# Kernel optimization log

Hardware: AMD Instinct MI355X
Metric: run time of the kernel (lower is better)

## Reference

```python
import jax, jax.numpy as jnp
import numpy as np

DT = 0.1
DN = ('NCHW', 'OIHW', 'NCHW')

LAP = jnp.array([[1., 2., 1.], [2., -12., 2.], [1., 2., 1.]], jnp.float32)
SOBEL_X = jnp.array([[-1., 0., 1.], [-2., 0., 2.], [-1., 0., 1.]], jnp.float32)
LAP_K = (LAP / 12.0)[None, None]  # [1,1,3,3], zero-padded laplacian kernel


def conv_lap(x):
    # 3x3 laplacian/12 conv with zero padding=1 on a single-channel map
    return jax.lax.conv_general_dilated(x, LAP_K, (1, 1), ((1, 1), (1, 1)), dimension_numbers=DN)


def conv1x1(x, w, b=None):
    # w: [O, C]
    y = jnp.einsum('bchw,oc->bohw', x, w)
    if b is not None:
        y = y + b[None, :, None, None]
    return y


def avg_pool5(x):
    # torch avg_pool2d(5,1,2) with count_include_pad=True -> always divide by 25
    s = jax.lax.reduce_window(x, 0.0, jax.lax.add, (1, 1, 5, 5), (1, 1, 1, 1),
                              [(0, 0), (0, 0), (2, 2), (2, 2)])
    return s / 25.0


def min_pool3(x):
    # -maxpool(-x) in torch == min-pool with +inf padding
    return jax.lax.reduce_window(x, jnp.inf, jax.lax.min, (1, 1, 3, 3), (1, 1, 1, 1),
                                 [(0, 0), (0, 0), (1, 1), (1, 1)])


def perception(x):
    # reduced_perception(x, 0): depthwise circular 3x3 conv with [sobel_x, sobel_x.T, lap]
    B, C, H, W = x.shape
    filters = jnp.stack([SOBEL_X, SOBEL_X.T, LAP])        # [3,3,3]
    k = jnp.tile(filters, (C, 1, 1))[:, None]              # [3C,1,3,3]; per-channel groups of 3
    xp = jnp.pad(x, ((0, 0), (0, 0), (1, 1), (1, 1)), mode='wrap')
    obs = jax.lax.conv_general_dilated(xp, k, (1, 1), 'VALID',
                                       feature_group_count=C, dimension_numbers=DN)
    return jnp.concatenate([x, obs], axis=1)               # [B, 4C, H, W]


def setup_inputs() -> dict:
    key = jax.random.key(0)
    ks = jax.random.split(key, 10)
    B, C, H, W = 16, 21, 256, 256
    hidden_n, gene_size = 96, 3
    return {
        'x': jax.random.uniform(ks[0], (B, C, H, W), jnp.float32),
        'rand_noise': jax.random.uniform(ks[1], (B, 1, H, W), jnp.float32),
        'w1_w': jax.random.normal(ks[2], (hidden_n, 4 * C), jnp.float32) * 0.05,
        'w1_b': jax.random.normal(ks[3], (hidden_n,), jnp.float32) * 0.02,
        'w2_w': jax.random.normal(ks[4], (gene_size, hidden_n), jnp.float32) * 0.05,
        'slow_w': jax.random.normal(ks[5], (3, 5), jnp.float32) * 0.1,
        'slow_b': jax.random.normal(ks[6], (3,), jnp.float32) * 0.02,
        'mod_w': jax.random.normal(ks[7], (3, 3), jnp.float32) * 0.1,
        'mod_b': jax.random.normal(ks[8], (3,), jnp.float32) * 0.02,
        'alpha': jnp.float32(0.1),
        'beta': jnp.float32(0.1),
        'omega': jnp.float32(0.0),
        'K': jnp.float32(0.5),
        'kappa': jnp.float32(0.5),
    }


def reference(x, rand_noise, w1_w, w1_b, w2_w, slow_w, slow_b, mod_w, mod_b,
              alpha, beta, omega, K, kappa):
    # step=0, k=4 -> slow (reaction-diffusion) branch executes; update_rate=0.5
    prefix = x[:, :12]
    gene = x[:, 12:15]
    a = x[:, 15:16]
    b = x[:, 16:17]
    d = x[:, 17:18]

    # slow_perception on rgba + hidden
    alpha_ch = x[:, 3:4]
    eroded = min_pool3(alpha_ch)
    Q = jnp.concatenate([alpha_ch, alpha_ch - eroded, conv_lap(alpha_ch), x[:, 4:6]], axis=1)  # 5 ch
    I = conv1x1(Q, slow_w, slow_b)
    Ia, Ib, Id = I[:, 0:1], I[:, 1:2], I[:, 2:3]

    # discrete reaction-diffusion update
    new_a = a + DT * (-alpha * a + omega * b + K * conv_lap(a) + Ia)
    new_b = b + DT * (-alpha * b - omega * a + K * conv_lap(b) + Ib)
    new_d = d + DT * (-beta * d + kappa * conv_lap(d) + Id)

    # local consensus update
    a_avg = avg_pool5(new_a)
    b_avg = avg_pool5(new_b)
    rho = jnp.sqrt(a_avg ** 2 + b_avg ** 2 + 1e-6)
    a_avg = a_avg / rho
    b_avg = b_avg / rho
    new_a = new_a + DT * (a_avg - new_a)
    new_b = new_b + DT * (b_avg - new_b)

    # ring attractor phases (variable naming follows the source's swapped unpack)
    phase = jnp.sqrt(new_a ** 2 + new_b ** 2 + 1e-6)  # local amplitude
    amplitude = jnp.arctan2(new_b, new_a)             # local angle
    a, b, d = new_a, new_b, new_d

    mod = conv1x1(jnp.concatenate([a, b, d], axis=1), mod_w, mod_b)

    # gene update MLP over full perception
    y = conv1x1(jax.nn.relu(conv1x1(perception(x), w1_w, w1_b)), w2_w)

    update_mask = jnp.floor(rand_noise + 0.5)
    xmp = jnp.pad(x[:, 3:4], ((0, 0), (0, 0), (1, 1), (1, 1)), mode='wrap')
    life = (jax.lax.reduce_window(xmp, -jnp.inf, jax.lax.max, (1, 1, 3, 3), (1, 1, 1, 1),
                                  'VALID') > 0.1).astype(x.dtype)
    new_gene = gene + y * update_mask * life

    x_final = jnp.concatenate([prefix, new_gene, a, b, d, mod], axis=1)
    return x_final, phase, amplitude
```

## Files before the change

### kernel.cpp

```cpp
#include <hip/hip_runtime.h>
#include <math.h>

#define HH 256
#define WW 256
#define CC 21
#define BB 16
#define HW (HH*WW)
#define CHW (CC*HW)
#define PHASE_OFF (BB*CHW)
#define AMP_OFF (PHASE_OFF + BB*HW)

static constexpr float DT = 0.1f;

typedef short short8 __attribute__((ext_vector_type(8)));
typedef float floatx4 __attribute__((ext_vector_type(4)));

__device__ __forceinline__ unsigned f2bf_bits(float f) {
    unsigned u = __builtin_bit_cast(unsigned, f);
    return (u + 0x7fffu + ((u >> 16) & 1u)) >> 16;
}
__device__ __forceinline__ float bf2f(short s) {
    unsigned u = ((unsigned)(unsigned short)s) << 16;
    return __builtin_bit_cast(float, u);
}

__global__ __launch_bounds__(256)
void k0_prep(const float* __restrict__ w1w, const float* __restrict__ w1b,
             const float* __restrict__ w2w,
             short* __restrict__ weff, float4* __restrict__ w2b)
{
    const float SX[9] = {-1.f, 0.f, 1.f, -2.f, 0.f, 2.f, -1.f, 0.f, 1.f};
    const float SY[9] = {-1.f, -2.f, -1.f, 0.f, 0.f, 0.f, 1.f, 2.f, 1.f};
    const float LP[9] = {1.f, 2.f, 1.f, 2.f, -12.f, 2.f, 1.f, 2.f, 1.f};
    const int i = blockIdx.x * 256 + threadIdx.x;
    if (i < 9 * 96 * 32) {
        const int s = i / (96 * 32);
        const int rem = i - s * 96 * 32;
        const int n = rem >> 5, c = rem & 31;
        float v = 0.f;
        if (c < 21) {
            v = w1w[n * 84 + c] * ((s == 4) ? 1.f : 0.f)
              + w1w[n * 84 + 21 + 3 * c + 0] * SX[s]
              + w1w[n * 84 + 21 + 3 * c + 1] * SY[s]
              + w1w[n * 84 + 21 + 3 * c + 2] * LP[s];
        }
        weff[i] = (short)f2bf_bits(v);
    } else if (i < 9 * 96 * 32 + 96) {
        const int n = i - 9 * 96 * 32;
        w2b[n] = make_float4(w2w[n], w2w[96 + n], w2w[192 + n], w1b[n]);
    }
}

__global__ __launch_bounds__(256)
void k12_react(const float* __restrict__ x,
               const float* __restrict__ slow_w, const float* __restrict__ slow_b,
               const float* __restrict__ mod_w, const float* __restrict__ mod_b,
               const float* __restrict__ alpha_p, const float* __restrict__ beta_p,
               const float* __restrict__ omega_p, const float* __restrict__ K_p,
               const float* __restrict__ kappa_p,
               float* __restrict__ out)
{
    __shared__ float t[6][14][38];
    __shared__ float na[12][36], nb[12][36];
    __shared__ float ha[12][32], hb[12][32];

    const int tx = threadIdx.x, ty = threadIdx.y;
    const int bb = blockIdx.z;
    const int X0 = blockIdx.x * 32, Y0 = blockIdx.y * 8;
    const int tid = ty * 32 + tx;

    const float alpha = alpha_p[0], beta = beta_p[0], omega = omega_p[0];
    const float Kc = K_p[0], kappa = kappa_p[0];

    const float* xb = x + (size_t)bb * CHW;
    for (int i = tid; i < 532; i += 256) {
        const int r = i / 38, c = i - r * 38;
        const int gy = Y0 + r - 3, gx = X0 + c - 3;
        const bool inb = (gy >= 0) && (gy < HH) && (gx >= 0) && (gx < WW);
        const int off = gy * WW + gx;
        t[0][r][c] = inb ? xb[3  * HW + off] : 0.f;
        t[1][r][c] = inb ? xb[4  * HW + off] : 0.f;
        t[2][r][c] = inb ? xb[5  * HW + off] : 0.f;
        t[3][r][c] = inb ? xb[15 * HW + off] : 0.f;
        t[4][r][c] = inb ? xb[16 * HW + off] : 0.f;
        t[5][r][c] = inb ? xb[17 * HW + off] : 0.f;
    }
    __syncthreads();

    for (int i = tid; i < 432; i += 256) {
        const int r2 = i / 36, c2 = i - r2 * 36;
        const int gy = Y0 + r2 - 2, gx = X0 + c2 - 2;
        float va = 0.f, vb = 0.f;
        if (gy >= 0 && gy < HH && gx >= 0 && gx < WW) {
            const int lr = r2 + 1, lc = c2 + 1;
            float lap3 = 0.f, lapA = 0.f, lapB = 0.f, emin = INFINITY;
            #pragma unroll
            for (int dy = -1; dy <= 1; dy++) {
                #pragma unroll
                for (int dx = -1; dx <= 1; dx++) {
                    const float lw = ((dy == 0 && dx == 0) ? -12.f
                                     : ((dy == 0 || dx == 0) ? 2.f : 1.f)) * (1.f / 12.f);
                    const float v3 = t[0][lr + dy][lc + dx];
                    lap3 = fmaf(lw, v3, lap3);
                    lapA = fmaf(lw, t[3][lr + dy][lc + dx], lapA);
                    lapB = fmaf(lw, t[4][lr + dy][lc + dx], lapB);
                    const bool nin = (gy + dy >= 0) && (gy + dy < HH) && (gx + dx >= 0) && (gx + dx < WW);
                    emin = fminf(emin, nin ? v3 : INFINITY);
                }
            }
            const float Q0 = t[0][lr][lc];
            const float Q1 = Q0 - emin, Q2 = lap3;
            const float Q3 = t[1][lr][lc], Q4 = t[2][lr][lc];
            const float I0 = slow_b[0] + slow_w[0] * Q0 + slow_w[1] * Q1 + slow_w[2] * Q2 + slow_w[3] * Q3 + slow_w[4] * Q4;
            const float I1 = slow_b[1] + slow_w[5] * Q0 + slow_w[6] * Q1 + slow_w[7] * Q2 + slow_w[8] * Q3 + slow_w[9] * Q4;
            const float a = t[3][lr][lc], b = t[4][lr][lc];
            va = a + DT * (-alpha * a + omega * b + Kc * lapA + I0);
            vb = b + DT * (-alpha * b - omega * a + Kc * lapB + I1);
        }
        na[r2][c2] = va;
        nb[r2][c2] = vb;
    }
    __syncthreads();

    for (int i = tid; i < 384; i += 256) {
        const int r = i >> 5, c = i & 31;
        float sa = 0.f, sb = 0.f;
        #pragma unroll
        for (int dx = 0; dx < 5; dx++) { sa += na[r][c + dx]; sb += nb[r][c + dx]; }
        ha[r][c] = sa; hb[r][c] = sb;
    }
    __syncthreads();

    const int gy = Y0 + ty, gx = X0 + tx;
    const int lr = ty + 3, lc = tx + 3;

    float sa = 0.f, sb = 0.f;
    #pragma unroll
    for (int dy = 0; dy < 5; dy++) { sa += ha[ty + dy][tx]; sb += hb[ty + dy][tx]; }
    sa *= (1.f / 25.f); sb *= (1.f / 25.f);
    const float rho = sqrtf(sa * sa + sb * sb + 1e-6f);
    const float an = sa / rho, bn = sb / rho;
    const float a0 = na[ty + 2][tx + 2], b0 = nb[ty + 2][tx + 2];
    const float A2 = a0 + DT * (an - a0);
    const float B2 = b0 + DT * (bn - b0);

    float lapD = 0.f, lap3 = 0.f, emin = INFINITY;
    #pragma unroll
    for (int dy = -1; dy <= 1; dy++)
        #pragma unroll
        for (int dx = -1; dx <= 1; dx++) {
            const float lw = ((dy == 0 && dx == 0) ? -12.f
                             : ((dy == 0 || dx == 0) ? 2.f : 1.f)) * (1.f / 12.f);
            lapD = fmaf(lw, t[5][lr + dy][lc + dx], lapD);
            const float v3 = t[0][lr + dy][lc + dx];
            lap3 = fmaf(lw, v3, lap3);
            const bool nin = (gy + dy >= 0) && (gy + dy < HH) && (gx + dx >= 0) && (gx + dx < WW);
            emin = fminf(emin, nin ? v3 : INFINITY);
        }
    const float Q0 = t[0][lr][lc];
    const float I2 = slow_b[2] + slow_w[10] * Q0 + slow_w[11] * (Q0 - emin) + slow_w[12] * lap3
                   + slow_w[13] * t[1][lr][lc] + slow_w[14] * t[2][lr][lc];
    const float d0 = t[5][lr][lc];
    const float nd = d0 + DT * (-beta * d0 + kappa * lapD + I2);

    const float ph = sqrtf(A2 * A2 + B2 * B2 + 1e-6f);
    const float am = atan2f(B2, A2);

    const int po = gy * WW + gx;
    float* ob = out + bb * CHW;
    ob[15 * HW + po] = A2;
    ob[16 * HW + po] = B2;
    ob[17 * HW + po] = nd;
    #pragma unroll
    for (int j = 0; j < 3; j++)
        ob[(18 + j) * HW + po] = mod_b[j] + mod_w[j * 3 + 0] * A2 + mod_w[j * 3 + 1] * B2 + mod_w[j * 3 + 2] * nd;
    out[PHASE_OFF + bb * HW + po] = ph;
    out[AMP_OFF + bb * HW + po] = am;
}

__global__ __launch_bounds__(256, 3)
void k3_gene(const float* __restrict__ x, const float* __restrict__ noise,
             const short* __restrict__ weff, const float4* __restrict__ w2b,
             float* __restrict__ out)
{
    __shared__ __align__(16) short xt[10][34][40];

    const int tx = threadIdx.x, ty = threadIdx.y;
    const int tid = ty * 32 + tx;
    const int w = tid >> 6, lane = tid & 63;
    const int ln = lane & 15, kg = lane >> 4;
    const int bb = blockIdx.z;
    const int X0 = blockIdx.x * 32, Y0 = blockIdx.y * 8;
    const float* xb = x + bb * CHW;

    for (int idx = tid; idx < 340; idx += 256) {
        const int r = idx / 34, cc = idx - r * 34;
        const int gy = (Y0 + r - 1) & (HH - 1);
        const int gxx = (X0 + cc - 1) & (WW - 1);
        const float* src = xb + gy * WW + gxx;
        short* dst = &xt[r][cc][0];
        #pragma unroll
        for (int c = 0; c < 20; c += 2) {
            const unsigned lo = f2bf_bits(src[c * HW]);
            const unsigned hi = f2bf_bits(src[(c + 1) * HW]);
            *(unsigned*)(dst + c) = lo | (hi << 16);
        }
        *(unsigned*)(dst + 20) = f2bf_bits(src[20 * HW]);
        #pragma unroll
        for (int c = 22; c < 40; c += 2) *(unsigned*)(dst + c) = 0u;
    }
    __syncthreads();

    const int gy = Y0 + ty, gx = X0 + tx;
    const int po = gy * WW + gx;
    float* ob = out + bb * CHW;
    const float* xc = xb + po;
    #pragma unroll
    for (int c = 0; c < 12; c++) ob[c * HW + po] = xc[c * HW];
    const float c12 = xc[12 * HW], c13 = xc[13 * HW], c14 = xc[14 * HW];

    float m = -1e30f;
    #pragma unroll
    for (int ky = 0; ky < 3; ky++)
        #pragma unroll
        for (int kx = 0; kx < 3; kx++)
            m = fmaxf(m, bf2f(xt[ty + ky][tx + kx][3]));
    const float life = (m > 0.1f) ? 1.f : 0.f;
    const float g = floorf(noise[bb * HW + po] + 0.5f) * life;

    const short* xtf = &xt[0][0][0];
    int aoff[4];
    #pragma unroll
    for (int mt = 0; mt < 4; mt++)
        aoff[mt] = ((2 * w + (mt >> 1)) * 34 + (mt & 1) * 16 + ln) * 40 + kg * 8;

    float yj0[4] = {0.f, 0.f, 0.f, 0.f};
    float yj1[4] = {0.f, 0.f, 0.f, 0.f};
    float yj2[4] = {0.f, 0.f, 0.f, 0.f};

    #pragma unroll
    for (int pass = 0; pass < 2; pass++) {
        floatx4 acc[4][3];
        #pragma unroll
        for (int mt = 0; mt < 4; mt++)
            #pragma unroll
            for (int nt = 0; nt < 3; nt++)
                acc[mt][nt] = (floatx4){0.f, 0.f, 0.f, 0.f};

        #pragma unroll
        for (int s = 0; s < 9; s++) {
            const int soff = ((s / 3) * 34 + (s % 3)) * 40;
            short8 af[4];
            #pragma unroll
            for (int mt = 0; mt < 4; mt++)
                af[mt] = *(const short8*)(xtf + aoff[mt] + soff);
            short8 bf[3];
            #pragma unroll
            for (int nt = 0; nt < 3; nt++)
                bf[nt] = *(const short8*)(weff + ((size_t)(s * 96 + pass * 48 + nt * 16 + ln)) * 32 + kg * 8);
            #pragma unroll
            for (int nt = 0; nt < 3; nt++)
                #pragma unroll
                for (int mt = 0; mt < 4; mt++)
                    acc[mt][nt] = __builtin_amdgcn_mfma_f32_16x16x32_bf16(bf[nt], af[mt], acc[mt][nt], 0, 0, 0);
        }

        #pragma unroll
        for (int nt = 0; nt < 3; nt++) {
            float4 wb[4];
            #pragma unroll
            for (int r = 0; r < 4; r++)
                wb[r] = w2b[pass * 48 + nt * 16 + kg * 4 + r];
            #pragma unroll
            for (int mt = 0; mt < 4; mt++)
                #pragma unroll
                for (int r = 0; r < 4; r++) {
                    const float h = fmaxf(acc[mt][nt][r] + wb[r].w, 0.f);
                    yj0[mt] = fmaf(h, wb[r].x, yj0[mt]);
                    yj1[mt] = fmaf(h, wb[r].y, yj1[mt]);
                    yj2[mt] = fmaf(h, wb[r].z, yj2[mt]);
                }
        }
    }

    float fy0 = 0.f, fy1 = 0.f, fy2 = 0.f;
    #pragma unroll
    for (int mt = 0; mt < 4; mt++) {
        float t0 = yj0[mt] + __shfl_xor(yj0[mt], 16, 64);
        t0 += __shfl_xor(t0, 32, 64);
        float t1 = yj1[mt] + __shfl_xor(yj1[mt], 16, 64);
        t1 += __shfl_xor(t1, 32, 64);
        float t2 = yj2[mt] + __shfl_xor(yj2[mt], 16, 64);
        t2 += __shfl_xor(t2, 32, 64);
        if (kg == mt) { fy0 = t0; fy1 = t1; fy2 = t2; }
    }

    ob[12 * HW + po] = c12 + fy0 * g;
    ob[13 * HW + po] = c13 + fy1 * g;
    ob[14 * HW + po] = c14 + fy2 * g;
}

extern "C" void kernel_launch(void* const* d_in, const int* in_sizes, int n_in,
                              void* d_out, int out_size, void* d_ws, size_t ws_size,
                              hipStream_t stream)
{
    const float* x      = (const float*)d_in[0];
    const float* noise  = (const float*)d_in[1];
    const float* w1w    = (const float*)d_in[2];
    const float* w1b    = (const float*)d_in[3];
    const float* w2w    = (const float*)d_in[4];
    const float* sloww  = (const float*)d_in[5];
    const float* slowb  = (const float*)d_in[6];
    const float* modw   = (const float*)d_in[7];
    const float* modb   = (const float*)d_in[8];
    const float* alphap = (const float*)d_in[9];
    const float* betap  = (const float*)d_in[10];
    const float* omegap = (const float*)d_in[11];
    const float* Kp     = (const float*)d_in[12];
    const float* kappap = (const float*)d_in[13];
    float* out = (float*)d_out;

    short* weff = (short*)d_ws;
    float4* w2b = (float4*)((char*)d_ws + 55296);

    dim3 blk(32, 8, 1);
    dim3 grd(WW / 32, HH / 8, BB);

    k0_prep<<<dim3(109), dim3(256), 0, stream>>>(w1w, w1b, w2w, weff, w2b);
    k12_react<<<grd, blk, 0, stream>>>(x, sloww, slowb, modw, modb,
                                       alphap, betap, omegap, Kp, kappap, out);
    k3_gene<<<grd, blk, 0, stream>>>(x, noise, weff, w2b, out);
}
```

Before: 307.0 us.

## Merge reaction and gene kernels into one launch with interleaved block roles

The separate reaction-diffusion and gene-MLP kernels become a single kernel. Even and odd blocks take the gene (MFMA) role and the reaction (stencil) role, and the two roles share shared memory through a union. The aim is to run the memory-bound stencil blocks alongside the compute-bound MFMA blocks on the same CUs, and to drop one kernel launch plus the tail gap between the two kernels. In exchange, the merged kernel runs under launch_bounds(256,3) and the reaction blocks allocate the larger union LDS footprint, which could limit occupancy.

```diff
diff --git a/kernel.cpp b/kernel.cpp
--- a/kernel.cpp
+++ b/kernel.cpp
@@ -51,253 +51,250 @@
     }
 }
 
-__global__ __launch_bounds__(256)
-void k12_react(const float* __restrict__ x,
-               const float* __restrict__ slow_w, const float* __restrict__ slow_b,
-               const float* __restrict__ mod_w, const float* __restrict__ mod_b,
-               const float* __restrict__ alpha_p, const float* __restrict__ beta_p,
-               const float* __restrict__ omega_p, const float* __restrict__ K_p,
-               const float* __restrict__ kappa_p,
-               float* __restrict__ out)
+union SMem {
+    short xt[10][34][40];
+    struct {
+        float t[6][14][38];
+        float na[12][36], nb[12][36];
+        float ha[12][32], hb[12][32];
+    } r;
+};
+
+__global__ __launch_bounds__(256, 3)
+void mega(const float* __restrict__ x, const float* __restrict__ noise,
+          const short* __restrict__ weff, const float4* __restrict__ w2b,
+          const float* __restrict__ slow_w, const float* __restrict__ slow_b,
+          const float* __restrict__ mod_w, const float* __restrict__ mod_b,
+          const float* __restrict__ alpha_p, const float* __restrict__ beta_p,
+          const float* __restrict__ omega_p, const float* __restrict__ K_p,
+          const float* __restrict__ kappa_p,
+          float* __restrict__ out)
 {
-    __shared__ float t[6][14][38];
-    __shared__ float na[12][36], nb[12][36];
-    __shared__ float ha[12][32], hb[12][32];
-
-    const int tx = threadIdx.x, ty = threadIdx.y;
-    const int bb = blockIdx.z;
-    const int X0 = blockIdx.x * 32, Y0 = blockIdx.y * 8;
-    const int tid = ty * 32 + tx;
-
-    const float alpha = alpha_p[0], beta = beta_p[0], omega = omega_p[0];
-    const float Kc = K_p[0], kappa = kappa_p[0];
-
-    const float* xb = x + (size_t)bb * CHW;
-    for (int i = tid; i < 532; i += 256) {
-        const int r = i / 38, c = i - r * 38;
-        const int gy = Y0 + r - 3, gx = X0 + c - 3;
-        const bool inb = (gy >= 0) && (gy < HH) && (gx >= 0) && (gx < WW);
-        const int off = gy * WW + gx;
-        t[0][r][c] = inb ? xb[3  * HW + off] : 0.f;
-        t[1][r][c] = inb ? xb[4  * HW + off] : 0.f;
-        t[2][r][c] = inb ? xb[5  * HW + off] : 0.f;
-        t[3][r][c] = inb ? xb[15 * HW + off] : 0.f;
-        t[4][r][c] = inb ? xb[16 * HW + off] : 0.f;
-        t[5][r][c] = inb ? xb[17 * HW + off] : 0.f;
-    }
-    __syncthreads();
-
-    for (int i = tid; i < 432; i += 256) {
-        const int r2 = i / 36, c2 = i - r2 * 36;
-        const int gy = Y0 + r2 - 2, gx = X0 + c2 - 2;
-        float va = 0.f, vb = 0.f;
-        if (gy >= 0 && gy < HH && gx >= 0 && gx < WW) {
-            const int lr = r2 + 1, lc = c2 + 1;
-            float lap3 = 0.f, lapA = 0.f, lapB = 0.f, emin = INFINITY;
-            #pragma unroll
-            for (int dy = -1; dy <= 1; dy++) {
-                #pragma unroll
-                for (int dx = -1; dx <= 1; dx++) {
-                    const float lw = ((dy == 0 && dx == 0) ? -12.f
-                                     : ((dy == 0 || dx == 0) ? 2.f : 1.f)) * (1.f / 12.f);
-                    const float v3 = t[0][lr + dy][lc + dx];
-                    lap3 = fmaf(lw, v3, lap3);
-                    lapA = fmaf(lw, t[3][lr + dy][lc + dx], lapA);
-                    lapB = fmaf(lw, t[4][lr + dy][lc + dx], lapB);
-                    const bool nin = (gy + dy >= 0) && (gy + dy < HH) && (gx + dx >= 0) && (gx + dx < WW);
-                    emin = fminf(emin, nin ? v3 : INFINITY);
-                }
-            }
-            const float Q0 = t[0][lr][lc];
-            const float Q1 = Q0 - emin, Q2 = lap3;
-            const float Q3 = t[1][lr][lc], Q4 = t[2][lr][lc];
-            const float I0 = slow_b[0] + slow_w[0] * Q0 + slow_w[1] * Q1 + slow_w[2] * Q2 + slow_w[3] * Q3 + slow_w[4] * Q4;
-            const float I1 = slow_b[1] + slow_w[5] * Q0 + slow_w[6] * Q1 + slow_w[7] * Q2 + slow_w[8] * Q3 + slow_w[9] * Q4;
-            const float a = t[3][lr][lc], b = t[4][lr][lc];
-            va = a + DT * (-alpha * a + omega * b + Kc * lapA + I0);
-            vb = b + DT * (-alpha * b - omega * a + Kc * lapB + I1);
-        }
-        na[r2][c2] = va;
-        nb[r2][c2] = vb;
-    }
-    __syncthreads();
-
-    for (int i = tid; i < 384; i += 256) {
-        const int r = i >> 5, c = i & 31;
-        float sa = 0.f, sb = 0.f;
-        #pragma unroll
-        for (int dx = 0; dx < 5; dx++) { sa += na[r][c + dx]; sb += nb[r][c + dx]; }
-        ha[r][c] = sa; hb[r][c] = sb;
-    }
-    __syncthreads();
-
-    const int gy = Y0 + ty, gx = X0 + tx;
-    const int lr = ty + 3, lc = tx + 3;
-
-    float sa = 0.f, sb = 0.f;
-    #pragma unroll
-    for (int dy = 0; dy < 5; dy++) { sa += ha[ty + dy][tx]; sb += hb[ty + dy][tx]; }
-    sa *= (1.f / 25.f); sb *= (1.f / 25.f);
-    const float rho = sqrtf(sa * sa + sb * sb + 1e-6f);
-    const float an = sa / rho, bn = sb / rho;
-    const float a0 = na[ty + 2][tx + 2], b0 = nb[ty + 2][tx + 2];
-    const float A2 = a0 + DT * (an - a0);
-    const float B2 = b0 + DT * (bn - b0);
-
-    float lapD = 0.f, lap3 = 0.f, emin = INFINITY;
-    #pragma unroll
-    for (int dy = -1; dy <= 1; dy++)
-        #pragma unroll
-        for (int dx = -1; dx <= 1; dx++) {
-            const float lw = ((dy == 0 && dx == 0) ? -12.f
-                             : ((dy == 0 || dx == 0) ? 2.f : 1.f)) * (1.f / 12.f);
-            lapD = fmaf(lw, t[5][lr + dy][lc + dx], lapD);
-            const float v3 = t[0][lr + dy][lc + dx];
-            lap3 = fmaf(lw, v3, lap3);
-            const bool nin = (gy + dy >= 0) && (gy + dy < HH) && (gx + dx >= 0) && (gx + dx < WW);
-            emin = fminf(emin, nin ? v3 : INFINITY);
-        }
-    const float Q0 = t[0][lr][lc];
-    const float I2 = slow_b[2] + slow_w[10] * Q0 + slow_w[11] * (Q0 - emin) + slow_w[12] * lap3
-                   + slow_w[13] * t[1][lr][lc] + slow_w[14] * t[2][lr][lc];
-    const float d0 = t[5][lr][lc];
-    const float nd = d0 + DT * (-beta * d0 + kappa * lapD + I2);
-
-    const float ph = sqrtf(A2 * A2 + B2 * B2 + 1e-6f);
-    const float am = atan2f(B2, A2);
-
-    const int po = gy * WW + gx;
-    float* ob = out + bb * CHW;
-    ob[15 * HW + po] = A2;
-    ob[16 * HW + po] = B2;
-    ob[17 * HW + po] = nd;
-    #pragma unroll
-    for (int j = 0; j < 3; j++)
-        ob[(18 + j) * HW + po] = mod_b[j] + mod_w[j * 3 + 0] * A2 + mod_w[j * 3 + 1] * B2 + mod_w[j * 3 + 2] * nd;
-    out[PHASE_OFF + bb * HW + po] = ph;
-    out[AMP_OFF + bb * HW + po] = am;
-}
-
-__global__ __launch_bounds__(256, 3)
-void k3_gene(const float* __restrict__ x, const float* __restrict__ noise,
-             const short* __restrict__ weff, const float4* __restrict__ w2b,
-             float* __restrict__ out)
-{
-    __shared__ __align__(16) short xt[10][34][40];
+    __shared__ SMem sm;
+
+    const int role = blockIdx.x & 1;
+    const int idx = blockIdx.x >> 1;
+    const int X0 = (idx & 7) * 32;
+    const int Y0 = ((idx >> 3) & 31) * 8;
+    const int bb = idx >> 8;
 
     const int tx = threadIdx.x, ty = threadIdx.y;
     const int tid = ty * 32 + tx;
-    const int w = tid >> 6, lane = tid & 63;
-    const int ln = lane & 15, kg = lane >> 4;
-    const int bb = blockIdx.z;
-    const int X0 = blockIdx.x * 32, Y0 = blockIdx.y * 8;
-    const float* xb = x + bb * CHW;
-
-    for (int idx = tid; idx < 340; idx += 256) {
-        const int r = idx / 34, cc = idx - r * 34;
-        const int gy = (Y0 + r - 1) & (HH - 1);
-        const int gxx = (X0 + cc - 1) & (WW - 1);
-        const float* src = xb + gy * WW + gxx;
-        short* dst = &xt[r][cc][0];
-        #pragma unroll
-        for (int c = 0; c < 20; c += 2) {
-            const unsigned lo = f2bf_bits(src[c * HW]);
-            const unsigned hi = f2bf_bits(src[(c + 1) * HW]);
-            *(unsigned*)(dst + c) = lo | (hi << 16);
-        }
-        *(unsigned*)(dst + 20) = f2bf_bits(src[20 * HW]);
-        #pragma unroll
-        for (int c = 22; c < 40; c += 2) *(unsigned*)(dst + c) = 0u;
-    }
-    __syncthreads();
-
+    const float* xb = x + (size_t)bb * CHW;
+    float* ob = out + (size_t)bb * CHW;
     const int gy = Y0 + ty, gx = X0 + tx;
     const int po = gy * WW + gx;
-    float* ob = out + bb * CHW;
-    const float* xc = xb + po;
-    #pragma unroll
-    for (int c = 0; c < 12; c++) ob[c * HW + po] = xc[c * HW];
-    const float c12 = xc[12 * HW], c13 = xc[13 * HW], c14 = xc[14 * HW];
-
-    float m = -1e30f;
-    #pragma unroll
-    for (int ky = 0; ky < 3; ky++)
-        #pragma unroll
-        for (int kx = 0; kx < 3; kx++)
-            m = fmaxf(m, bf2f(xt[ty + ky][tx + kx][3]));
-    const float life = (m > 0.1f) ? 1.f : 0.f;
-    const float g = floorf(noise[bb * HW + po] + 0.5f) * life;
-
-    const short* xtf = &xt[0][0][0];
-    int aoff[4];
-    #pragma unroll
-    for (int mt = 0; mt < 4; mt++)
-        aoff[mt] = ((2 * w + (mt >> 1)) * 34 + (mt & 1) * 16 + ln) * 40 + kg * 8;
-
-    float yj0[4] = {0.f, 0.f, 0.f, 0.f};
-    float yj1[4] = {0.f, 0.f, 0.f, 0.f};
-    float yj2[4] = {0.f, 0.f, 0.f, 0.f};
-
-    #pragma unroll
-    for (int pass = 0; pass < 2; pass++) {
-        floatx4 acc[4][3];
+
+    if (role == 0) {
+        const int w = tid >> 6, lane = tid & 63;
+        const int ln = lane & 15, kg = lane >> 4;
+
+        for (int i2 = tid; i2 < 340; i2 += 256) {
+            const int r = i2 / 34, cc = i2 - r * 34;
+            const int gyy = (Y0 + r - 1) & (HH - 1);
+            const int gxx = (X0 + cc - 1) & (WW - 1);
+            const float* src = xb + gyy * WW + gxx;
+            short* dst = &sm.xt[r][cc][0];
+            #pragma unroll
+            for (int c = 0; c < 20; c += 2) {
+                const unsigned lo = f2bf_bits(src[c * HW]);
+                const unsigned hi = f2bf_bits(src[(c + 1) * HW]);
+                *(unsigned*)(dst + c) = lo | (hi << 16);
+            }
+            *(unsigned*)(dst + 20) = f2bf_bits(src[20 * HW]);
+            #pragma unroll
+            for (int c = 22; c < 40; c += 2) *(unsigned*)(dst + c) = 0u;
+        }
+        __syncthreads();
+
+        const float* xc = xb + po;
+        #pragma unroll
+        for (int c = 0; c < 12; c++) ob[c * HW + po] = xc[c * HW];
+        const float c12 = xc[12 * HW], c13 = xc[13 * HW], c14 = xc[14 * HW];
+
+        float m = -1e30f;
+        #pragma unroll
+        for (int ky = 0; ky < 3; ky++)
+            #pragma unroll
+            for (int kx = 0; kx < 3; kx++)
+                m = fmaxf(m, bf2f(sm.xt[ty + ky][tx + kx][3]));
+        const float life = (m > 0.1f) ? 1.f : 0.f;
+        const float g = floorf(noise[bb * HW + po] + 0.5f) * life;
+
+        const short* xtf = &sm.xt[0][0][0];
+        int aoff[4];
         #pragma unroll
         for (int mt = 0; mt < 4; mt++)
-            #pragma unroll
-            for (int nt = 0; nt < 3; nt++)
-                acc[mt][nt] = (floatx4){0.f, 0.f, 0.f, 0.f};
-
-        #pragma unroll
-        for (int s = 0; s < 9; s++) {
-            const int soff = ((s / 3) * 34 + (s % 3)) * 40;
-            short8 af[4];
+            aoff[mt] = ((2 * w + (mt >> 1)) * 34 + (mt & 1) * 16 + ln) * 40 + kg * 8;
+
+        float yj0[4] = {0.f, 0.f, 0.f, 0.f};
+        float yj1[4] = {0.f, 0.f, 0.f, 0.f};
+        float yj2[4] = {0.f, 0.f, 0.f, 0.f};
+
+        #pragma unroll
+        for (int pass = 0; pass < 2; pass++) {
+            floatx4 acc[4][3];
             #pragma unroll
             for (int mt = 0; mt < 4; mt++)
-                af[mt] = *(const short8*)(xtf + aoff[mt] + soff);
-            short8 bf[3];
-            #pragma unroll
-            for (int nt = 0; nt < 3; nt++)
-                bf[nt] = *(const short8*)(weff + ((size_t)(s * 96 + pass * 48 + nt * 16 + ln)) * 32 + kg * 8);
-            #pragma unroll
-            for (int nt = 0; nt < 3; nt++)
+                #pragma unroll
+                for (int nt = 0; nt < 3; nt++)
+                    acc[mt][nt] = (floatx4){0.f, 0.f, 0.f, 0.f};
+
+            #pragma unroll
+            for (int s = 0; s < 9; s++) {
+                const int soff = ((s / 3) * 34 + (s % 3)) * 40;
+                short8 af[4];
                 #pragma unroll
                 for (int mt = 0; mt < 4; mt++)
-                    acc[mt][nt] = __builtin_amdgcn_mfma_f32_16x16x32_bf16(bf[nt], af[mt], acc[mt][nt], 0, 0, 0);
-        }
-
-        #pragma unroll
-        for (int nt = 0; nt < 3; nt++) {
-            float4 wb[4];
-            #pragma unroll
-            for (int r = 0; r < 4; r++)
-                wb[r] = w2b[pass * 48 + nt * 16 + kg * 4 + r];
-            #pragma unroll
-            for (int mt = 0; mt < 4; mt++)
-                #pragma unroll
-                for (int r = 0; r < 4; r++) {
-                    const float h = fmaxf(acc[mt][nt][r] + wb[r].w, 0.f);
-                    yj0[mt] = fmaf(h, wb[r].x, yj0[mt]);
-                    yj1[mt] = fmaf(h, wb[r].y, yj1[mt]);
-                    yj2[mt] = fmaf(h, wb[r].z, yj2[mt]);
+                    af[mt] = *(const short8*)(xtf + aoff[mt] + soff);
+                short8 bf[3];
+                #pragma unroll
+                for (int nt = 0; nt < 3; nt++)
+                    bf[nt] = *(const short8*)(weff + ((size_t)(s * 96 + pass * 48 + nt * 16 + ln)) * 32 + kg * 8);
+                #pragma unroll
+                for (int nt = 0; nt < 3; nt++)
+                    #pragma unroll
+                    for (int mt = 0; mt < 4; mt++)
+                        acc[mt][nt] = __builtin_amdgcn_mfma_f32_16x16x32_bf16(bf[nt], af[mt], acc[mt][nt], 0, 0, 0);
+            }
+
+            #pragma unroll
+            for (int nt = 0; nt < 3; nt++) {
+                float4 wb[4];
+                #pragma unroll
+                for (int r = 0; r < 4; r++)
+                    wb[r] = w2b[pass * 48 + nt * 16 + kg * 4 + r];
+                #pragma unroll
+                for (int mt = 0; mt < 4; mt++)
+                    #pragma unroll
+                    for (int r = 0; r < 4; r++) {
+                        const float h = fmaxf(acc[mt][nt][r] + wb[r].w, 0.f);
+                        yj0[mt] = fmaf(h, wb[r].x, yj0[mt]);
+                        yj1[mt] = fmaf(h, wb[r].y, yj1[mt]);
+                        yj2[mt] = fmaf(h, wb[r].z, yj2[mt]);
+                    }
+            }
+        }
+
+        float fy0 = 0.f, fy1 = 0.f, fy2 = 0.f;
+        #pragma unroll
+        for (int mt = 0; mt < 4; mt++) {
+            float t0 = yj0[mt] + __shfl_xor(yj0[mt], 16, 64);
+            t0 += __shfl_xor(t0, 32, 64);
+            float t1 = yj1[mt] + __shfl_xor(yj1[mt], 16, 64);
+            t1 += __shfl_xor(t1, 32, 64);
+            float t2 = yj2[mt] + __shfl_xor(yj2[mt], 16, 64);
+            t2 += __shfl_xor(t2, 32, 64);
+            if (kg == mt) { fy0 = t0; fy1 = t1; fy2 = t2; }
+        }
+
+        ob[12 * HW + po] = c12 + fy0 * g;
+        ob[13 * HW + po] = c13 + fy1 * g;
+        ob[14 * HW + po] = c14 + fy2 * g;
+    } else {
+        const float alpha = alpha_p[0], beta = beta_p[0], omega = omega_p[0];
+        const float Kc = K_p[0], kappa = kappa_p[0];
+
+        for (int i = tid; i < 532; i += 256) {
+            const int r = i / 38, c = i - r * 38;
+            const int gyy = Y0 + r - 3, gxx = X0 + c - 3;
+            const bool inb = (gyy >= 0) && (gyy < HH) && (gxx >= 0) && (gxx < WW);
+            const int off = gyy * WW + gxx;
+            sm.r.t[0][r][c] = inb ? xb[3  * HW + off] : 0.f;
+            sm.r.t[1][r][c] = inb ? xb[4  * HW + off] : 0.f;
+            sm.r.t[2][r][c] = inb ? xb[5  * HW + off] : 0.f;
+            sm.r.t[3][r][c] = inb ? xb[15 * HW + off] : 0.f;
+            sm.r.t[4][r][c] = inb ? xb[16 * HW + off] : 0.f;
+            sm.r.t[5][r][c] = inb ? xb[17 * HW + off] : 0.f;
+        }
+        __syncthreads();
+
+        for (int i = tid; i < 432; i += 256) {
+            const int r2 = i / 36, c2 = i - r2 * 36;
+            const int gyy = Y0 + r2 - 2, gxx = X0 + c2 - 2;
+            float va = 0.f, vb = 0.f;
+            if (gyy >= 0 && gyy < HH && gxx >= 0 && gxx < WW) {
+                const int lr = r2 + 1, lc = c2 + 1;
+                float lap3 = 0.f, lapA = 0.f, lapB = 0.f, emin = INFINITY;
+                #pragma unroll
+                for (int dy = -1; dy <= 1; dy++) {
+                    #pragma unroll
+                    for (int dx = -1; dx <= 1; dx++) {
+                        const float lw = ((dy == 0 && dx == 0) ? -12.f
+                                         : ((dy == 0 || dx == 0) ? 2.f : 1.f)) * (1.f / 12.f);
+                        const float v3 = sm.r.t[0][lr + dy][lc + dx];
+                        lap3 = fmaf(lw, v3, lap3);
+                        lapA = fmaf(lw, sm.r.t[3][lr + dy][lc + dx], lapA);
+                        lapB = fmaf(lw, sm.r.t[4][lr + dy][lc + dx], lapB);
+                        const bool nin = (gyy + dy >= 0) && (gyy + dy < HH) && (gxx + dx >= 0) && (gxx + dx < WW);
+                        emin = fminf(emin, nin ? v3 : INFINITY);
+                    }
                 }
-        }
+                const float Q0 = sm.r.t[0][lr][lc];
+                const float Q1 = Q0 - emin, Q2 = lap3;
+                const float Q3 = sm.r.t[1][lr][lc], Q4 = sm.r.t[2][lr][lc];
+                const float I0 = slow_b[0] + slow_w[0] * Q0 + slow_w[1] * Q1 + slow_w[2] * Q2 + slow_w[3] * Q3 + slow_w[4] * Q4;
+                const float I1 = slow_b[1] + slow_w[5] * Q0 + slow_w[6] * Q1 + slow_w[7] * Q2 + slow_w[8] * Q3 + slow_w[9] * Q4;
+                const float a = sm.r.t[3][lr][lc], b = sm.r.t[4][lr][lc];
+                va = a + DT * (-alpha * a + omega * b + Kc * lapA + I0);
+                vb = b + DT * (-alpha * b - omega * a + Kc * lapB + I1);
+            }
+            sm.r.na[r2][c2] = va;
+            sm.r.nb[r2][c2] = vb;
+        }
+        __syncthreads();
+
+        for (int i = tid; i < 384; i += 256) {
+            const int r = i >> 5, c = i & 31;
+            float sa = 0.f, sb = 0.f;
+            #pragma unroll
+            for (int dx = 0; dx < 5; dx++) { sa += sm.r.na[r][c + dx]; sb += sm.r.nb[r][c + dx]; }
+            sm.r.ha[r][c] = sa; sm.r.hb[r][c] = sb;
+        }
+        __syncthreads();
+
+        const int lr = ty + 3, lc = tx + 3;
+        float sa = 0.f, sb = 0.f;
+        #pragma unroll
+        for (int dy = 0; dy < 5; dy++) { sa += sm.r.ha[ty + dy][tx]; sb += sm.r.hb[ty + dy][tx]; }
+        sa *= (1.f / 25.f); sb *= (1.f / 25.f);
+        const float rho = sqrtf(sa * sa + sb * sb + 1e-6f);
+        const float an = sa / rho, bn = sb / rho;
+        const float a0 = sm.r.na[ty + 2][tx + 2], b0 = sm.r.nb[ty + 2][tx + 2];
+        const float A2 = a0 + DT * (an - a0);
+        const float B2 = b0 + DT * (bn - b0);
+
+        float lapD = 0.f, lap3 = 0.f, emin = INFINITY;
+        #pragma unroll
+        for (int dy = -1; dy <= 1; dy++)
+            #pragma unroll
+            for (int dx = -1; dx <= 1; dx++) {
+                const float lw = ((dy == 0 && dx == 0) ? -12.f
+                                 : ((dy == 0 || dx == 0) ? 2.f : 1.f)) * (1.f / 12.f);
+                lapD = fmaf(lw, sm.r.t[5][lr + dy][lc + dx], lapD);
+                const float v3 = sm.r.t[0][lr + dy][lc + dx];
+                lap3 = fmaf(lw, v3, lap3);
+                const bool nin = (gy + dy >= 0) && (gy + dy < HH) && (gx + dx >= 0) && (gx + dx < WW);
+                emin = fminf(emin, nin ? v3 : INFINITY);
+            }
+        const float Q0 = sm.r.t[0][lr][lc];
+        const float I2 = slow_b[2] + slow_w[10] * Q0 + slow_w[11] * (Q0 - emin) + slow_w[12] * lap3
+                       + slow_w[13] * sm.r.t[1][lr][lc] + slow_w[14] * sm.r.t[2][lr][lc];
+        const float d0 = sm.r.t[5][lr][lc];
+        const float nd = d0 + DT * (-beta * d0 + kappa * lapD + I2);
+
+        const float ph = sqrtf(A2 * A2 + B2 * B2 + 1e-6f);
+        const float am = atan2f(B2, A2);
+
+        ob[15 * HW + po] = A2;
+        ob[16 * HW + po] = B2;
+        ob[17 * HW + po] = nd;
+        #pragma unroll
+        for (int j = 0; j < 3; j++)
+            ob[(18 + j) * HW + po] = mod_b[j] + mod_w[j * 3 + 0] * A2 + mod_w[j * 3 + 1] * B2 + mod_w[j * 3 + 2] * nd;
+        out[PHASE_OFF + bb * HW + po] = ph;
+        out[AMP_OFF + bb * HW + po] = am;
     }
-
-    float fy0 = 0.f, fy1 = 0.f, fy2 = 0.f;
-    #pragma unroll
-    for (int mt = 0; mt < 4; mt++) {
-        float t0 = yj0[mt] + __shfl_xor(yj0[mt], 16, 64);
-        t0 += __shfl_xor(t0, 32, 64);
-        float t1 = yj1[mt] + __shfl_xor(yj1[mt], 16, 64);
-        t1 += __shfl_xor(t1, 32, 64);
-        float t2 = yj2[mt] + __shfl_xor(yj2[mt], 16, 64);
-        t2 += __shfl_xor(t2, 32, 64);
-        if (kg == mt) { fy0 = t0; fy1 = t1; fy2 = t2; }
-    }
-
-    ob[12 * HW + po] = c12 + fy0 * g;
-    ob[13 * HW + po] = c13 + fy1 * g;
-    ob[14 * HW + po] = c14 + fy2 * g;
 }
 
 extern "C" void kernel_launch(void* const* d_in, const int* in_sizes, int n_in,
@@ -323,11 +320,8 @@
     short* weff = (short*)d_ws;
     float4* w2b = (float4*)((char*)d_ws + 55296);
 
-    dim3 blk(32, 8, 1);
-    dim3 grd(WW / 32, HH / 8, BB);
-
     k0_prep<<<dim3(109), dim3(256), 0, stream>>>(w1w, w1b, w2w, weff, w2b);
-    k12_react<<<grd, blk, 0, stream>>>(x, sloww, slowb, modw, modb,
-                                       alphap, betap, omegap, Kp, kappap, out);
-    k3_gene<<<grd, blk, 0, stream>>>(x, noise, weff, w2b, out);
-}
+    mega<<<dim3(8192), dim3(32, 8, 1), 0, stream>>>(x, noise, weff, w2b,
+                                                    sloww, slowb, modw, modb,
+                                                    alphap, betap, omegap, Kp, kappap, out);
+}
```

New measurement: 381.5 us. 24.2% more time.

## Pre-pack input into pixel-major bf16 buffer for gene kernel tile loads

Applied to the files above, without the earlier changes.

Adds a pack kernel that reads all 21 channels per pixel once, copies the 12 prefix channels to the output, and writes a pixel-major bf16 record of 24 shorts into workspace. The gene kernel then fills its shared-memory halo tile with 16-byte vector loads from this packed buffer, instead of strided per-channel fp32 loads with conversion, which were repeated for every halo pixel. The cost is an extra kernel launch plus a write and re-read of a roughly 50 MB intermediate, in exchange for fewer redundant halo reads and uncoalesced channel-strided accesses.

```diff
diff --git a/kernel.cpp b/kernel.cpp
--- a/kernel.cpp
+++ b/kernel.cpp
@@ -9,6 +9,7 @@
 #define CHW (CC*HW)
 #define PHASE_OFF (BB*CHW)
 #define AMP_OFF (PHASE_OFF + BB*HW)
+#define XPC 24
 
 static constexpr float DT = 0.1f;
 
@@ -49,6 +50,34 @@
         const int n = i - 9 * 96 * 32;
         w2b[n] = make_float4(w2w[n], w2w[96 + n], w2w[192 + n], w1b[n]);
     }
+}
+
+__global__ __launch_bounds__(256)
+void kp_pack(const float* __restrict__ x, short* __restrict__ xp,
+             float* __restrict__ out)
+{
+    const int pix = blockIdx.x * 256 + threadIdx.x;
+    const int bb = pix >> 16;
+    const int pi = pix & (HW - 1);
+    const float* xb = x + (size_t)bb * CHW + pi;
+    float* ob = out + (size_t)bb * CHW + pi;
+
+    float v[21];
+    #pragma unroll
+    for (int c = 0; c < 21; c++) v[c] = xb[c * HW];
+    #pragma unroll
+    for (int c = 0; c < 12; c++) ob[c * HW] = v[c];
+
+    unsigned rec[12];
+    #pragma unroll
+    for (int c = 0; c < 20; c += 2)
+        rec[c >> 1] = f2bf_bits(v[c]) | (f2bf_bits(v[c + 1]) << 16);
+    rec[10] = f2bf_bits(v[20]);
+    rec[11] = 0u;
+    uint4* dst = (uint4*)(xp + (size_t)pix * XPC);
+    dst[0] = make_uint4(rec[0], rec[1], rec[2], rec[3]);
+    dst[1] = make_uint4(rec[4], rec[5], rec[6], rec[7]);
+    dst[2] = make_uint4(rec[8], rec[9], rec[10], rec[11]);
 }
 
 __global__ __launch_bounds__(256)
@@ -167,7 +196,7 @@
     const float am = atan2f(B2, A2);
 
     const int po = gy * WW + gx;
-    float* ob = out + bb * CHW;
+    float* ob = out + (size_t)bb * CHW;
     ob[15 * HW + po] = A2;
     ob[16 * HW + po] = B2;
     ob[17 * HW + po] = nd;
@@ -179,7 +208,8 @@
 }
 
 __global__ __launch_bounds__(256, 3)
-void k3_gene(const float* __restrict__ x, const float* __restrict__ noise,
+void k3_gene(const float* __restrict__ x, const short* __restrict__ xp,
+             const float* __restrict__ noise,
              const short* __restrict__ weff, const float4* __restrict__ w2b,
              float* __restrict__ out)
 {
@@ -191,32 +221,28 @@
     const int ln = lane & 15, kg = lane >> 4;
     const int bb = blockIdx.z;
     const int X0 = blockIdx.x * 32, Y0 = blockIdx.y * 8;
-    const float* xb = x + bb * CHW;
-
-    for (int idx = tid; idx < 340; idx += 256) {
-        const int r = idx / 34, cc = idx - r * 34;
-        const int gy = (Y0 + r - 1) & (HH - 1);
-        const int gxx = (X0 + cc - 1) & (WW - 1);
-        const float* src = xb + gy * WW + gxx;
-        short* dst = &xt[r][cc][0];
-        #pragma unroll
-        for (int c = 0; c < 20; c += 2) {
-            const unsigned lo = f2bf_bits(src[c * HW]);
-            const unsigned hi = f2bf_bits(src[(c + 1) * HW]);
-            *(unsigned*)(dst + c) = lo | (hi << 16);
-        }
-        *(unsigned*)(dst + 20) = f2bf_bits(src[20 * HW]);
-        #pragma unroll
-        for (int c = 22; c < 40; c += 2) *(unsigned*)(dst + c) = 0u;
+
+    #pragma unroll
+    for (int it = 0; it < 2; it++) {
+        const int idx = tid + it * 256;
+        if (idx < 340) {
+            const int r = idx / 34, cc = idx - r * 34;
+            const int gyy = (Y0 + r - 1) & (HH - 1);
+            const int gxx = (X0 + cc - 1) & (WW - 1);
+            const uint4* src = (const uint4*)(xp + ((size_t)(bb << 16) + gyy * WW + gxx) * XPC);
+            uint4* dst = (uint4*)&xt[r][cc][0];
+            dst[0] = src[0];
+            dst[1] = src[1];
+            dst[2] = src[2];
+            dst[3] = make_uint4(0u, 0u, 0u, 0u);
+        }
     }
     __syncthreads();
 
     const int gy = Y0 + ty, gx = X0 + tx;
     const int po = gy * WW + gx;
-    float* ob = out + bb * CHW;
-    const float* xc = xb + po;
-    #pragma unroll
-    for (int c = 0; c < 12; c++) ob[c * HW + po] = xc[c * HW];
+    float* ob = out + (size_t)bb * CHW;
+    const float* xc = x + (size_t)bb * CHW + po;
     const float c12 = xc[12 * HW], c13 = xc[13 * HW], c14 = xc[14 * HW];
 
     float m = -1e30f;
@@ -322,12 +348,14 @@
 
     short* weff = (short*)d_ws;
     float4* w2b = (float4*)((char*)d_ws + 55296);
+    short* xp   = (short*)((char*)d_ws + 57344);
 
     dim3 blk(32, 8, 1);
     dim3 grd(WW / 32, HH / 8, BB);
 
     k0_prep<<<dim3(109), dim3(256), 0, stream>>>(w1w, w1b, w2w, weff, w2b);
+    kp_pack<<<dim3(BB * HW / 256), dim3(256), 0, stream>>>(x, xp, out);
     k12_react<<<grd, blk, 0, stream>>>(x, sloww, slowb, modw, modb,
                                        alphap, betap, omegap, Kp, kappap, out);
-    k3_gene<<<grd, blk, 0, stream>>>(x, noise, weff, w2b, out);
-}
+    k3_gene<<<grd, blk, 0, stream>>>(x, xp, noise, weff, w2b, out);
+}
```

Result: slower. 317.6 us (+3.5%).
